# Kernel optimization log

Hardware: AMD Instinct MI355X
Metric: run time of the kernel (lower is better)

## Reference

```python
import jax, jax.numpy as jnp
import numpy as np

D, HEADS, HD, L, P, DFF = 256, 8, 32, 4, 4, 2048
B, NQ = 4, 900
SHAPES = [(128, 128), (64, 64), (32, 32), (16, 16)]
S = sum(h * w for h, w in SHAPES)


def setup_inputs():
    ks = iter(jax.random.split(jax.random.key(0), 20))
    rn = lambda *s: jax.random.normal(next(ks), s, jnp.float32) * 0.02
    cxcy = jax.random.uniform(next(ks), (B, NQ, 1, 2), minval=0.1, maxval=0.9)
    wh = jax.random.uniform(next(ks), (B, NQ, 1, 2), minval=0.05, maxval=0.3)
    ref = jnp.broadcast_to(jnp.concatenate([cxcy, wh], -1), (B, NQ, L, 4))
    starts = np.cumsum([0] + [h * w for h, w in SHAPES[:-1]])
    return dict(
        query=jax.random.normal(next(ks), (B, NQ, D), jnp.float32),
        query_pos=jax.random.normal(next(ks), (B, NQ, D), jnp.float32),
        reference_points=ref,
        input_flatten=jax.random.normal(next(ks), (B, S, D), jnp.float32),
        input_spatial_shapes=jnp.array(SHAPES, jnp.int32),
        input_level_start_index=jnp.array(starts, jnp.int32),
        sa_in_w=rn(3, D, D), sa_in_b=jnp.zeros((3, D)),
        sa_out_w=rn(D, D), sa_out_b=jnp.zeros((D,)),
        norm1_g=jnp.ones((D,)), norm1_b=jnp.zeros((D,)),
        value_w=rn(D, D), value_b=jnp.zeros((D,)),
        off_w=rn(D, HEADS * L * P * 2),
        off_b=jax.random.uniform(next(ks), (HEADS * L * P * 2,), minval=-1.0, maxval=1.0),
        aw_w=rn(D, HEADS * L * P), aw_b=jnp.zeros((HEADS * L * P,)),
        ca_out_w=rn(D, D), ca_out_b=jnp.zeros((D,)),
        norm2_g=jnp.ones((D,)), norm2_b=jnp.zeros((D,)),
        lin1_w=rn(D, DFF), lin1_b=jnp.zeros((DFF,)),
        lin2_w=rn(DFF, D), lin2_b=jnp.zeros((D,)),
        norm3_g=jnp.ones((D,)), norm3_b=jnp.zeros((D,)),
    )


def _ln(x, g, b, eps=1e-5):
    m = x.mean(-1, keepdims=True)
    v = ((x - m) ** 2).mean(-1, keepdims=True)
    return (x - m) * jax.lax.rsqrt(v + eps) * g + b


def _msdeform(q, input_flatten, ref, shapes, starts, value_w, value_b,
              off_w, off_b, aw_w, aw_b, out_w, out_b):
    Bq, Nq, _ = q.shape
    # value: (B, heads, S, head_dim)
    v = (input_flatten @ value_w + value_b).reshape(Bq, -1, HEADS, HD).transpose(0, 2, 1, 3)
    off = (q @ off_w + off_b).reshape(Bq, Nq, HEADS, L, P, 2).transpose(0, 2, 1, 3, 4, 5)
    aw = jax.nn.softmax((q @ aw_w + aw_b).reshape(Bq, Nq, HEADS, L * P), axis=-1)
    aw = aw.reshape(Bq, Nq, HEADS, L, P).transpose(0, 2, 1, 3, 4)  # (B,H,Nq,L,P)
    refc = ref[:, None, :, :, None, :]  # (B,1,Nq,L,1,4)
    # box refs: center + offset/P * wh * 0.5  (Deformable-DETR convention)
    loc = refc[..., :2] + off / P * refc[..., 2:] * 0.5  # (B,H,Nq,L,P,2)
    out = jnp.zeros((Bq, HEADS, Nq, HD), q.dtype)
    for l, (H, W) in enumerate(shapes):
        vl = jax.lax.dynamic_slice_in_dim(v, starts[l], H * W, axis=2)  # (B,H,HW,hd)
        x = loc[:, :, :, l, :, 0] * W - 0.5  # align_corners=False pixel coords
        y = loc[:, :, :, l, :, 1] * H - 0.5
        x0, y0 = jnp.floor(x), jnp.floor(y)
        dx, dy = x - x0, y - y0

        def g(xi, yi):
            valid = (xi >= 0) & (xi < W) & (yi >= 0) & (yi < H)  # zero padding
            idx = (jnp.clip(yi, 0, H - 1) * W + jnp.clip(xi, 0, W - 1)).astype(jnp.int32)
            gat = jnp.take_along_axis(vl, idx.reshape(Bq, HEADS, Nq * P, 1), axis=2)
            return gat.reshape(Bq, HEADS, Nq, P, HD) * valid[..., None]

        samp = (((1 - dx) * (1 - dy))[..., None] * g(x0, y0)
                + (dx * (1 - dy))[..., None] * g(x0 + 1, y0)
                + ((1 - dx) * dy)[..., None] * g(x0, y0 + 1)
                + (dx * dy)[..., None] * g(x0 + 1, y0 + 1))
        out = out + jnp.sum(aw[:, :, :, l, :, None] * samp, axis=3)
    return out.transpose(0, 2, 1, 3).reshape(Bq, Nq, D) @ out_w + out_b


def _layer(query, query_pos, reference_points, input_flatten, shapes, starts, p):
    Bq, Nq, _ = query.shape
    qk = query + query_pos
    heads = lambda x: x.reshape(Bq, Nq, HEADS, HD).transpose(0, 2, 1, 3)
    qh = heads(qk @ p['sa_in_w'][0] + p['sa_in_b'][0])
    kh = heads(qk @ p['sa_in_w'][1] + p['sa_in_b'][1])
    vh = heads(query @ p['sa_in_w'][2] + p['sa_in_b'][2])
    attn = jax.nn.softmax(jnp.einsum('bhqd,bhkd->bhqk', qh, kh) * (HD ** -0.5), axis=-1)
    sa = jnp.einsum('bhqk,bhkd->bhqd', attn, vh).transpose(0, 2, 1, 3).reshape(Bq, Nq, D)
    sa = sa @ p['sa_out_w'] + p['sa_out_b']
    x = _ln(query + sa, p['norm1_g'], p['norm1_b'])
    ca = _msdeform(x + query_pos, input_flatten, reference_points, shapes, starts,
                   p['value_w'], p['value_b'], p['off_w'], p['off_b'],
                   p['aw_w'], p['aw_b'], p['ca_out_w'], p['ca_out_b'])
    x = _ln(x + ca, p['norm2_g'], p['norm2_b'])
    ffn = jax.nn.relu(x @ p['lin1_w'] + p['lin1_b']) @ p['lin2_w'] + p['lin2_b']
    return _ln(x + ffn, p['norm3_g'], p['norm3_b'])


PNAMES = ['sa_in_w', 'sa_in_b', 'sa_out_w', 'sa_out_b', 'norm1_g', 'norm1_b',
          'value_w', 'value_b', 'off_w', 'off_b', 'aw_w', 'aw_b',
          'ca_out_w', 'ca_out_b', 'norm2_g', 'norm2_b',
          'lin1_w', 'lin1_b', 'lin2_w', 'lin2_b', 'norm3_g', 'norm3_b']


def reference(query, query_pos, reference_points, input_flatten,
              input_spatial_shapes, input_level_start_index,
              sa_in_w, sa_in_b, sa_out_w, sa_out_b, norm1_g, norm1_b,
              value_w, value_b, off_w, off_b, aw_w, aw_b,
              ca_out_w, ca_out_b, norm2_g, norm2_b,
              lin1_w, lin1_b, lin2_w, lin2_b, norm3_g, norm3_b):
    # spatial shapes / start indices are static structural metadata
    shapes = [(int(h), int(w)) for h, w in np.asarray(input_spatial_shapes)]
    starts = [int(s) for s in np.asarray(input_level_start_index)]
    p = dict(zip(PNAMES, (sa_in_w, sa_in_b, sa_out_w, sa_out_b, norm1_g, norm1_b,
                          value_w, value_b, off_w, off_b, aw_w, aw_b,
                          ca_out_w, ca_out_b, norm2_g, norm2_b,
                          lin1_w, lin1_b, lin2_w, lin2_b, norm3_g, norm3_b)))
    return _layer(query, query_pos, reference_points, input_flatten, shapes, starts, p)
```

## Files before the change

kernel.cpp:

```cpp
#include <hip/hip_runtime.h>
#include <hip/hip_bf16.h>

#define DD   256
#define NH   8
#define HDIM 32
#define LV   4
#define NP   4
#define DFF  2048
#define BB   4
#define NQQ  900
#define SS   21760

typedef __bf16 bf16x8 __attribute__((ext_vector_type(8)));
typedef __bf16 bf16x2 __attribute__((ext_vector_type(2)));
typedef float  f32x4  __attribute__((ext_vector_type(4)));

__device__ inline void stval(float* p, float v) { *p = v; }
__device__ inline void stval(__bf16* p, float v) { *p = (__bf16)v; }

__device__ __forceinline__ void gload16(const void* g, void* l) {
    __builtin_amdgcn_global_load_lds(
        (const __attribute__((address_space(1))) void*)g,
        (__attribute__((address_space(3))) void*)l, 16, 0, 0);
}

struct TPtrs {
    const float* s[10];
    __bf16* d[10];
};

__global__ void transp_all(TPtrs P) {
    const int Ks[10] = {256, 256, 256, 256, 256, 256, 256, 256, 256, 2048};
    const int Ns[10] = {256, 256, 256, 256, 256, 256, 128, 256, 2048, 256};
    const int tiles[10] = {64, 64, 64, 64, 64, 64, 32, 64, 512, 512};
    int t = blockIdx.x;
    int j = 0, base = 0;
    while (t >= base + tiles[j]) { base += tiles[j]; j++; }
    int lt = t - base;
    int K = Ks[j], N = Ns[j];
    int tn = N >> 5;
    int nb = (lt % tn) * 32, kb = (lt / tn) * 32;
    const float* W = P.s[j];
    __bf16* Wt = P.d[j];
    __shared__ float tbuf[32][33];
    for (int i = threadIdx.y; i < 32; i += 8)
        tbuf[i][threadIdx.x] = W[(size_t)(kb + i) * N + nb + threadIdx.x];
    __syncthreads();
    for (int i = threadIdx.y; i < 32; i += 8)
        Wt[(size_t)(nb + i) * K + kb + threadIdx.x] = (__bf16)tbuf[threadIdx.x][i];
}

#define BM 64
#define BN 64
#define BKK 64

template <typename AT, typename OT, int RELU, int NSUB, bool LNF>
__device__ __forceinline__ void gemm_body(
    int bx, int by, char* ldsraw,
    const AT* __restrict__ A, const float* __restrict__ A2,
    const __bf16* __restrict__ Wt,
    const float* __restrict__ bias, const float* __restrict__ bias2, int nsplit,
    const float* __restrict__ res, const float* __restrict__ lng,
    const float* __restrict__ lnb,
    OT* __restrict__ C, int M, int N, int K) {
    int tid = threadIdx.x;
    int lane = tid & 63;
    int wave = tid >> 6;
    int wr = wave >> 1, wc = wave & 1;
    int m0 = by * BM;
    int n0 = bx * (BN * NSUB);

    __bf16* As = (__bf16*)ldsraw;
    __bf16* Bs = (__bf16*)(ldsraw + BM * BKK * 2);
    float* rsum  = (float*)(ldsraw + BM * BKK * 2 + NSUB * BN * BKK * 2);
    float* rsum2 = rsum + 128;

    f32x4 acc[NSUB][2][2] = {};

    int srow = tid >> 2;
    int sq = tid & 3;
    int u0 = sq << 1;
    int p0 = (u0 ^ (srow & 7)) * 8;
    int p1 = ((u0 + 1) ^ (srow & 7)) * 8;
    int fr = lane & 15, gq = lane >> 4;

    for (int k0 = 0; k0 < K; k0 += BKK) {
        {
            int gm = m0 + srow;
            bf16x8 v0 = {}, v1 = {};
            if (gm < M) {
                if constexpr (sizeof(AT) == 4) {
                    const float* ap = (const float*)A + (size_t)gm * K + k0 + sq * 16;
                    f32x4 f0 = *(const f32x4*)(ap + 0);
                    f32x4 f1 = *(const f32x4*)(ap + 4);
                    f32x4 f2 = *(const f32x4*)(ap + 8);
                    f32x4 f3 = *(const f32x4*)(ap + 12);
                    if (A2) {
                        const float* ap2 = A2 + (size_t)gm * K + k0 + sq * 16;
                        f0 += *(const f32x4*)(ap2 + 0);
                        f1 += *(const f32x4*)(ap2 + 4);
                        f2 += *(const f32x4*)(ap2 + 8);
                        f3 += *(const f32x4*)(ap2 + 12);
                    }
#pragma unroll
                    for (int e = 0; e < 4; e++) {
                        v0[e] = (__bf16)f0[e]; v0[e + 4] = (__bf16)f1[e];
                        v1[e] = (__bf16)f2[e]; v1[e + 4] = (__bf16)f3[e];
                    }
                } else {
                    const __bf16* ap = (const __bf16*)A + (size_t)gm * K + k0 + sq * 16;
                    v0 = *(const bf16x8*)(ap);
                    v1 = *(const bf16x8*)(ap + 8);
                }
            }
            *(bf16x8*)(&As[srow * 64 + p0]) = v0;
            *(bf16x8*)(&As[srow * 64 + p1]) = v1;
        }
#pragma unroll
        for (int ns = 0; ns < NSUB; ns++) {
            int gn = n0 + ns * BN + srow;
            const __bf16* bp = Wt + (size_t)gn * K + k0 + sq * 16;
            bf16x8 w0 = *(const bf16x8*)(bp);
            bf16x8 w1 = *(const bf16x8*)(bp + 8);
            *(bf16x8*)(&Bs[ns * BN * BKK + srow * 64 + p0]) = w0;
            *(bf16x8*)(&Bs[ns * BN * BKK + srow * 64 + p1]) = w1;
        }
        __syncthreads();
#pragma unroll
        for (int ks = 0; ks < 2; ks++) {
            bf16x8 a[2];
#pragma unroll
            for (int i = 0; i < 2; i++) {
                int ma = wr * 32 + i * 16 + fr;
                a[i] = *(const bf16x8*)(&As[ma * 64 + ((ks * 4 + gq) ^ (ma & 7)) * 8]);
            }
#pragma unroll
            for (int ns = 0; ns < NSUB; ns++) {
                bf16x8 b[2];
#pragma unroll
                for (int j = 0; j < 2; j++) {
                    int nb = wc * 32 + j * 16 + fr;
                    b[j] = *(const bf16x8*)(&Bs[ns * BN * BKK + nb * 64 + ((ks * 4 + gq) ^ (nb & 7)) * 8]);
                }
#pragma unroll
                for (int i = 0; i < 2; i++)
#pragma unroll
                    for (int j = 0; j < 2; j++)
                        acc[ns][i][j] = __builtin_amdgcn_mfma_f32_16x16x32_bf16(a[i], b[j], acc[ns][i][j], 0, 0, 0);
            }
        }
        __syncthreads();
    }
    int orow = gq * 4;
    if constexpr (!LNF) {
#pragma unroll
        for (int ns = 0; ns < NSUB; ns++)
#pragma unroll
            for (int i = 0; i < 2; i++)
#pragma unroll
                for (int j = 0; j < 2; j++) {
                    int gn = n0 + ns * BN + wc * 32 + j * 16 + fr;
                    float bv = (gn < nsplit) ? bias[gn] : bias2[gn - nsplit];
#pragma unroll
                    for (int r = 0; r < 4; r++) {
                        int gm = m0 + wr * 32 + i * 16 + orow + r;
                        if (gm < M) {
                            float v = acc[ns][i][j][r] + bv;
                            if (RELU) v = fmaxf(v, 0.f);
                            stval(C + (size_t)gm * N + gn, v);
                        }
                    }
                }
    } else {
        float part[2][4] = {};
#pragma unroll
        for (int ns = 0; ns < NSUB; ns++)
#pragma unroll
            for (int i = 0; i < 2; i++)
#pragma unroll
                for (int j = 0; j < 2; j++) {
                    int gn = ns * BN + wc * 32 + j * 16 + fr;
                    float bv = bias[gn];
#pragma unroll
                    for (int r = 0; r < 4; r++) {
                        int gm = m0 + wr * 32 + i * 16 + orow + r;
                        float rv = (gm < M) ? res[(size_t)gm * 256 + gn] : 0.f;
                        float x = acc[ns][i][j][r] + bv + rv;
                        acc[ns][i][j][r] = x;
                        part[i][r] += x;
                    }
                }
#pragma unroll
        for (int i = 0; i < 2; i++)
#pragma unroll
            for (int r = 0; r < 4; r++) {
                float v = part[i][r];
                v += __shfl_xor(v, 1);
                v += __shfl_xor(v, 2);
                v += __shfl_xor(v, 4);
                v += __shfl_xor(v, 8);
                part[i][r] = v;
            }
        if (fr == 0) {
#pragma unroll
            for (int i = 0; i < 2; i++)
#pragma unroll
                for (int r = 0; r < 4; r++)
                    rsum[(wr * 32 + i * 16 + orow + r) * 2 + wc] = part[i][r];
        }
        __syncthreads();
        float mean[2][4];
#pragma unroll
        for (int i = 0; i < 2; i++)
#pragma unroll
            for (int r = 0; r < 4; r++) {
                int rl = wr * 32 + i * 16 + orow + r;
                mean[i][r] = (rsum[rl * 2] + rsum[rl * 2 + 1]) * (1.f / 256.f);
            }
        float p2[2][4] = {};
#pragma unroll
        for (int ns = 0; ns < NSUB; ns++)
#pragma unroll
            for (int i = 0; i < 2; i++)
#pragma unroll
                for (int j = 0; j < 2; j++)
#pragma unroll
                    for (int r = 0; r < 4; r++) {
                        float d = acc[ns][i][j][r] - mean[i][r];
                        p2[i][r] += d * d;
                    }
#pragma unroll
        for (int i = 0; i < 2; i++)
#pragma unroll
            for (int r = 0; r < 4; r++) {
                float v = p2[i][r];
                v += __shfl_xor(v, 1);
                v += __shfl_xor(v, 2);
                v += __shfl_xor(v, 4);
                v += __shfl_xor(v, 8);
                p2[i][r] = v;
            }
        if (fr == 0) {
#pragma unroll
            for (int i = 0; i < 2; i++)
#pragma unroll
                for (int r = 0; r < 4; r++)
                    rsum2[(wr * 32 + i * 16 + orow + r) * 2 + wc] = p2[i][r];
        }
        __syncthreads();
        float rstd[2][4];
#pragma unroll
        for (int i = 0; i < 2; i++)
#pragma unroll
            for (int r = 0; r < 4; r++) {
                int rl = wr * 32 + i * 16 + orow + r;
                float var = (rsum2[rl * 2] + rsum2[rl * 2 + 1]) * (1.f / 256.f);
                rstd[i][r] = rsqrtf(var + 1e-5f);
            }
#pragma unroll
        for (int ns = 0; ns < NSUB; ns++)
#pragma unroll
            for (int i = 0; i < 2; i++)
#pragma unroll
                for (int j = 0; j < 2; j++) {
                    int gn = ns * BN + wc * 32 + j * 16 + fr;
                    float gv = lng[gn], bev = lnb[gn];
#pragma unroll
                    for (int r = 0; r < 4; r++) {
                        int gm = m0 + wr * 32 + i * 16 + orow + r;
                        if (gm < M) {
                            float y = (acc[ns][i][j][r] - mean[i][r]) * rstd[i][r] * gv + bev;
                            stval(C + (size_t)gm * 256 + gn, y);
                        }
                    }
                }
    }
}

template <typename AT, typename OT, int RELU, int NSUB, bool LNF>
__global__ __launch_bounds__(256) void mfma_gemm(
    const AT* __restrict__ A, const float* __restrict__ A2,
    const __bf16* __restrict__ Wt,
    const float* __restrict__ bias, const float* __restrict__ bias2, int nsplit,
    const float* __restrict__ res, const float* __restrict__ lng,
    const float* __restrict__ lnb,
    OT* __restrict__ C, int M, int N, int K) {
    __shared__ __attribute__((aligned(16))) char lds[BM * BKK * 2 + NSUB * BN * BKK * 2 + (LNF ? 1024 : 0)];
    gemm_body<AT, OT, RELU, NSUB, LNF>(blockIdx.x, blockIdx.y, lds, A, A2, Wt,
                                       bias, bias2, nsplit, res, lng, lnb, C, M, N, K);
}

__device__ __forceinline__ void value_body(
    int bx, char* ldsraw,
    const float* __restrict__ A, const __bf16* __restrict__ Wt,
    const float* __restrict__ bias, __bf16* __restrict__ C) {
    int tid = threadIdx.x;
    int lane = tid & 63;
    int wave = tid >> 6;
    int fr = lane & 15, gq = lane >> 4;
    int m0 = bx * 64;

    __bf16* As = (__bf16*)ldsraw;
    __bf16* Bq = (__bf16*)(ldsraw + 16384);

    f32x4 acc[4][4] = {};

    int srow = tid >> 2;
    int sq = tid & 3;
    int u0 = sq << 1;
    int p0 = (u0 ^ (srow & 7)) * 8;
    int p1 = ((u0 + 1) ^ (srow & 7)) * 8;

    int c_row = lane >> 3;
    int c_u = lane & 7;
    int gu = c_u ^ c_row;
    const __bf16* bsrc0 = Wt + (size_t)(wave * 64 + c_row) * 256 + gu * 8;
    const float* aptr = A + (size_t)(m0 + srow) * 256 + sq * 16;

    f32x4 fa0 = *(const f32x4*)(aptr + 0);
    f32x4 fa1 = *(const f32x4*)(aptr + 4);
    f32x4 fa2 = *(const f32x4*)(aptr + 8);
    f32x4 fa3 = *(const f32x4*)(aptr + 12);
    __builtin_amdgcn_sched_barrier(0);
#pragma unroll
    for (int c = 0; c < 8; c++)
        gload16(bsrc0 + (size_t)c * 8 * 256, &Bq[wave * 4096 + c * 512]);
    asm volatile("s_waitcnt vmcnt(8)" ::: "memory");
    __builtin_amdgcn_sched_barrier(0);
    {
        bf16x8 v0, v1;
#pragma unroll
        for (int e = 0; e < 4; e++) {
            v0[e] = (__bf16)fa0[e]; v0[e + 4] = (__bf16)fa1[e];
            v1[e] = (__bf16)fa2[e]; v1[e + 4] = (__bf16)fa3[e];
        }
        *(bf16x8*)(&As[srow * 64 + p0]) = v0;
        *(bf16x8*)(&As[srow * 64 + p1]) = v1;
    }
    asm volatile("s_waitcnt lgkmcnt(0)" ::: "memory");
    __builtin_amdgcn_s_barrier();

#pragma unroll
    for (int step = 0; step < 4; step++) {
        int p = step & 1;
        if (step < 3) {
            const float* ap2 = aptr + (step + 1) * 64;
            fa0 = *(const f32x4*)(ap2 + 0);
            fa1 = *(const f32x4*)(ap2 + 4);
            fa2 = *(const f32x4*)(ap2 + 8);
            fa3 = *(const f32x4*)(ap2 + 12);
            __builtin_amdgcn_sched_barrier(0);
            const __bf16* bsrc = bsrc0 + (step + 1) * 64;
#pragma unroll
            for (int c = 0; c < 8; c++)
                gload16(bsrc + (size_t)c * 8 * 256, &Bq[((p ^ 1) * 4 + wave) * 4096 + c * 512]);
            asm volatile("s_waitcnt vmcnt(12)" ::: "memory");
        } else {
            asm volatile("s_waitcnt vmcnt(0)" ::: "memory");
        }
        __builtin_amdgcn_sched_barrier(0);
#pragma unroll
        for (int ks = 0; ks < 2; ks++) {
            bf16x8 a[4], b[4];
#pragma unroll
            for (int i = 0; i < 4; i++) {
                int ma = i * 16 + fr;
                a[i] = *(const bf16x8*)(&As[p * 4096 + ma * 64 + ((ks * 4 + gq) ^ (ma & 7)) * 8]);
                b[i] = *(const bf16x8*)(&Bq[(p * 4 + wave) * 4096 + ma * 64 + ((ks * 4 + gq) ^ (ma & 7)) * 8]);
            }
#pragma unroll
            for (int i = 0; i < 4; i++)
#pragma unroll
                for (int j = 0; j < 4; j++)
                    acc[i][j] = __builtin_amdgcn_mfma_f32_16x16x32_bf16(a[i], b[j], acc[i][j], 0, 0, 0);
        }
        if (step < 3) {
            asm volatile("s_waitcnt vmcnt(8)" ::: "memory");
            __builtin_amdgcn_sched_barrier(0);
            bf16x8 v0, v1;
#pragma unroll
            for (int e = 0; e < 4; e++) {
                v0[e] = (__bf16)fa0[e]; v0[e + 4] = (__bf16)fa1[e];
                v1[e] = (__bf16)fa2[e]; v1[e + 4] = (__bf16)fa3[e];
            }
            *(bf16x8*)(&As[(p ^ 1) * 4096 + srow * 64 + p0]) = v0;
            *(bf16x8*)(&As[(p ^ 1) * 4096 + srow * 64 + p1]) = v1;
            asm volatile("s_waitcnt lgkmcnt(0)" ::: "memory");
            __builtin_amdgcn_s_barrier();
        }
    }

#pragma unroll
    for (int i = 0; i < 4; i++)
#pragma unroll
        for (int j = 0; j < 4; j++) {
            int gn = wave * 64 + j * 16 + fr;
            float bv = bias[gn];
#pragma unroll
            for (int r = 0; r < 4; r++) {
                int gm = m0 + i * 16 + gq * 4 + r;
                C[(size_t)gm * 256 + gn] = (__bf16)(acc[i][j][r] + bv);
            }
        }
}

#define NVALB 1360
#define NQKB  228
#define NVB   228

__global__ __launch_bounds__(256) void fused_head(
    const float* __restrict__ input_flat, const __bf16* __restrict__ wt_val,
    const float* __restrict__ value_b, __bf16* __restrict__ vbig,
    const float* __restrict__ query, const float* __restrict__ query_pos,
    const __bf16* __restrict__ wt_q, const float* __restrict__ sa_in_b,
    __bf16* __restrict__ qkbuf, const __bf16* __restrict__ wt_v,
    __bf16* __restrict__ Vp, int M) {
    __shared__ __attribute__((aligned(16))) char lds[81920];
    int bx = blockIdx.x;
    if (bx < NVALB) {
        value_body(bx, lds, input_flat, wt_val, value_b, vbig);
    } else if (bx < NVALB + NQKB) {
        int b2 = bx - NVALB;
        gemm_body<float, __bf16, 0, 2, false>(b2 & 3, b2 >> 2, lds,
            query, query_pos, wt_q, sa_in_b, sa_in_b, 1 << 30,
            nullptr, nullptr, nullptr, qkbuf, M, 512, 256);
    } else {
        int b2 = bx - NVALB - NQKB;
        gemm_body<float, __bf16, 0, 1, false>(b2 & 3, b2 >> 2, lds,
            query, nullptr, wt_v, sa_in_b + 512, sa_in_b, 1 << 30,
            nullptr, nullptr, nullptr, Vp, M, 256, 256);
    }
}

__global__ void fillmark(float* o, int n, float v) {
    int i = blockIdx.x * blockDim.x + threadIdx.x;
    if (i < n) o[i] = v;
}

__global__ void ln_res(const float* a, const float* b,
                       const float* g, const float* be, float* o) {
    int row = blockIdx.x;
    int t = threadIdx.x;
    float x = a[(size_t)row * DD + t] + b[(size_t)row * DD + t];
    __shared__ float red[DD];
    red[t] = x;
    __syncthreads();
    for (int s = 128; s > 0; s >>= 1) {
        if (t < s) red[t] += red[t + s];
        __syncthreads();
    }
    float m = red[0] * (1.f / DD);
    __syncthreads();
    float d0 = x - m;
    red[t] = d0 * d0;
    __syncthreads();
    for (int s = 128; s > 0; s >>= 1) {
        if (t < s) red[t] += red[t + s];
        __syncthreads();
    }
    float v = red[0] * (1.f / DD);
    o[(size_t)row * DD + t] = d0 * rsqrtf(v + 1e-5f) * g[t] + be[t];
}

#define QT 64
#define KT 64
#define NT ((NQQ + KT - 1) / KT)
#define QKLD 512

__global__ __launch_bounds__(256) void sa_attn_mfma(
    const __bf16* __restrict__ QK, const __bf16* __restrict__ V,
    float* __restrict__ O) {
    int blk = blockIdx.x;
    int tq = blk % NT;
    int bh = blk / NT;
    int h = bh % NH;
    int b = bh / NH;
    int tid = threadIdx.x;
    int lane = tid & 63;
    int wave = tid >> 6;
    int fr = lane & 15, gq = lane >> 4;
    int q0 = tq * QT;

    __shared__ __attribute__((aligned(16))) __bf16 Ks[KT][56];
    __shared__ __attribute__((aligned(16))) __bf16 Vt[HDIM][72];
    __shared__ __attribute__((aligned(16))) __bf16 Ps[4][16][72];

    int qrow = q0 + wave * 16 + fr;
    bf16x8 aq = {};
    if (qrow < NQQ)
        aq = *(const bf16x8*)(QK + ((size_t)(b * NQQ + qrow)) * QKLD + h * HDIM + gq * 8);

    f32x4 o0 = {}, o1 = {};
    float m_r[4] = {-1e30f, -1e30f, -1e30f, -1e30f};
    float l_r[4] = {0.f, 0.f, 0.f, 0.f};
    const float scale = 0.17677669529663687f;

    for (int kt = 0; kt < NT; kt++) {
        int kv0 = kt * KT;
        {
            int r = tid >> 2;
            int c8 = (tid & 3) * 8;
            int kvr = kv0 + r;
            bf16x8 kv_ = {}, vv_ = {};
            if (kvr < NQQ) {
                kv_ = *(const bf16x8*)(QK + ((size_t)(b * NQQ + kvr)) * QKLD + 256 + h * HDIM + c8);
                vv_ = *(const bf16x8*)(V + ((size_t)(b * NQQ + kvr)) * DD + h * HDIM + c8);
            }
            *(bf16x8*)(&Ks[r][c8]) = kv_;
#pragma unroll
            for (int j = 0; j < 8; j++) Vt[c8 + j][r] = vv_[j];
        }
        __syncthreads();

        f32x4 s[4];
#pragma unroll
        for (int f = 0; f < 4; f++) {
            bf16x8 bk = *(const bf16x8*)(&Ks[f * 16 + fr][gq * 8]);
            f32x4 z = {};
            s[f] = __builtin_amdgcn_mfma_f32_16x16x32_bf16(aq, bk, z, 0, 0, 0);
        }
#pragma unroll
        for (int f = 0; f < 4; f++) {
            bool valid = (kv0 + f * 16 + fr) < NQQ;
#pragma unroll
            for (int r = 0; r < 4; r++)
                s[f][r] = valid ? s[f][r] * scale : -1e30f;
        }
        float sc_[4];
#pragma unroll
        for (int r = 0; r < 4; r++) {
            float v = fmaxf(fmaxf(s[0][r], s[1][r]), fmaxf(s[2][r], s[3][r]));
            v = fmaxf(v, __shfl_xor(v, 1));
            v = fmaxf(v, __shfl_xor(v, 2));
            v = fmaxf(v, __shfl_xor(v, 4));
            v = fmaxf(v, __shfl_xor(v, 8));
            float mn = fmaxf(m_r[r], v);
            sc_[r] = expf(m_r[r] - mn);
            m_r[r] = mn;
        }
        float rs[4] = {0.f, 0.f, 0.f, 0.f};
#pragma unroll
        for (int f = 0; f < 4; f++)
#pragma unroll
            for (int r = 0; r < 4; r++) {
                float e = expf(s[f][r] - m_r[r]);
                s[f][r] = e;
                rs[r] += e;
            }
#pragma unroll
        for (int r = 0; r < 4; r++) {
            float v = rs[r];
            v += __shfl_xor(v, 1);
            v += __shfl_xor(v, 2);
            v += __shfl_xor(v, 4);
            v += __shfl_xor(v, 8);
            l_r[r] = l_r[r] * sc_[r] + v;
            o0[r] *= sc_[r];
            o1[r] *= sc_[r];
        }
#pragma unroll
        for (int f = 0; f < 4; f++)
#pragma unroll
            for (int r = 0; r < 4; r++)
                Ps[wave][gq * 4 + r][f * 16 + fr] = (__bf16)s[f][r];
#pragma unroll
        for (int c = 0; c < 2; c++) {
            bf16x8 ap = *(const bf16x8*)(&Ps[wave][fr][c * 32 + gq * 8]);
            bf16x8 bv0 = *(const bf16x8*)(&Vt[fr][c * 32 + gq * 8]);
            bf16x8 bv1 = *(const bf16x8*)(&Vt[16 + fr][c * 32 + gq * 8]);
            o0 = __builtin_amdgcn_mfma_f32_16x16x32_bf16(ap, bv0, o0, 0, 0, 0);
            o1 = __builtin_amdgcn_mfma_f32_16x16x32_bf16(ap, bv1, o1, 0, 0, 0);
        }
        __syncthreads();
    }
#pragma unroll
    for (int r = 0; r < 4; r++) {
        int qr = q0 + wave * 16 + gq * 4 + r;
        if (qr < NQQ) {
            float inv = 1.f / l_r[r];
            O[((size_t)(b * NQQ + qr)) * DD + h * HDIM + fr] = o0[r] * inv;
            O[((size_t)(b * NQQ + qr)) * DD + h * HDIM + 16 + fr] = o1[r] * inv;
        }
    }
}

#define OAW 384

__global__ __launch_bounds__(256) void msdeform3(
    const __bf16* __restrict__ val, const __bf16* __restrict__ oa,
    const float* __restrict__ ref, float* __restrict__ out) {
    int tid = threadIdx.x;
    int row = blockIdx.x;
    int b_ = row / NQQ;

    __shared__ float sx[128], sy[128], sw[128];

    if (tid < 128) {
        int h = tid >> 4;
        int lp = tid & 15;
        int l = lp >> 2;
        float logit = (float)oa[(size_t)row * OAW + 256 + h * 16 + lp];
        float ox = (float)oa[(size_t)row * OAW + h * 32 + lp * 2];
        float oy = (float)oa[(size_t)row * OAW + h * 32 + lp * 2 + 1];
        const float* rp = ref + ((size_t)row * LV + l) * 4;
        float cx = rp[0], cy = rp[1], rw = rp[2], rh = rp[3];
        float mv = logit;
        mv = fmaxf(mv, __shfl_xor(mv, 1));
        mv = fmaxf(mv, __shfl_xor(mv, 2));
        mv = fmaxf(mv, __shfl_xor(mv, 4));
        mv = fmaxf(mv, __shfl_xor(mv, 8));
        float e = expf(logit - mv);
        float sum = e;
        sum += __shfl_xor(sum, 1);
        sum += __shfl_xor(sum, 2);
        sum += __shfl_xor(sum, 4);
        sum += __shfl_xor(sum, 8);
        int Wl = 128 >> l;
        float lx = cx + ox * (1.0f / NP) * rw * 0.5f;
        float ly = cy + oy * (1.0f / NP) * rh * 0.5f;
        sx[tid] = lx * Wl - 0.5f;
        sy[tid] = ly * Wl - 0.5f;
        sw[tid] = e / sum;
    }
    __syncthreads();

    int cpar = tid & 7;
    int dgrp = (tid >> 3) & 3;
    int h = tid >> 5;
    const int stt[4] = {0, 16384, 20480, 21504};
    const __bf16* vb = val + (size_t)b_ * SS * DD + h * HDIM + dgrp * 8;
    float facc[8] = {};
#pragma unroll
    for (int k = 0; k < 8; k++) {
        int combo = cpar * 8 + k;
        int lp = combo >> 2;
        int tap = combo & 3;
        int l = lp >> 2;
        int Wl = 128 >> l;
        int cidx = h * 16 + lp;
        float x = sx[cidx], y = sy[cidx], w = sw[cidx];
        float x0f = floorf(x), y0f = floorf(y);
        float dx = x - x0f, dy = y - y0f;
        int xi = (int)x0f + (tap & 1);
        int yi = (int)y0f + (tap >> 1);
        float wt = ((tap & 1) ? dx : 1.f - dx) * ((tap >> 1) ? dy : 1.f - dy) * w;
        if ((xi >= 0) & (xi < Wl) & (yi >= 0) & (yi < Wl)) {
            bf16x8 t = *(const bf16x8*)(vb + (size_t)(stt[l] + yi * Wl + xi) * DD);
#pragma unroll
            for (int e = 0; e < 8; e++) facc[e] += wt * (float)t[e];
        }
    }
#pragma unroll
    for (int e = 0; e < 8; e++) {
        facc[e] += __shfl_xor(facc[e], 1);
        facc[e] += __shfl_xor(facc[e], 2);
        facc[e] += __shfl_xor(facc[e], 4);
    }
    float v = facc[0];
#pragma unroll
    for (int e = 1; e < 8; e++) if (cpar == e) v = facc[e];
    out[(size_t)row * DD + tid] = v;
}

extern "C" void kernel_launch(void* const* d_in, const int* in_sizes, int n_in,
                              void* d_out, int out_size, void* d_ws, size_t ws_size,
                              hipStream_t stream) {
    const float* query      = (const float*)d_in[0];
    const float* query_pos  = (const float*)d_in[1];
    const float* refpts     = (const float*)d_in[2];
    const float* input_flat = (const float*)d_in[3];
    const float* sa_in_w    = (const float*)d_in[6];
    const float* sa_in_b    = (const float*)d_in[7];
    const float* sa_out_w   = (const float*)d_in[8];
    const float* sa_out_b   = (const float*)d_in[9];
    const float* norm1_g    = (const float*)d_in[10];
    const float* norm1_b    = (const float*)d_in[11];
    const float* value_w    = (const float*)d_in[12];
    const float* value_b    = (const float*)d_in[13];
    const float* off_w      = (const float*)d_in[14];
    const float* off_b      = (const float*)d_in[15];
    const float* aw_w       = (const float*)d_in[16];
    const float* aw_b       = (const float*)d_in[17];
    const float* ca_out_w   = (const float*)d_in[18];
    const float* ca_out_b   = (const float*)d_in[19];
    const float* norm2_g    = (const float*)d_in[20];
    const float* norm2_b    = (const float*)d_in[21];
    const float* lin1_w     = (const float*)d_in[22];
    const float* lin1_b     = (const float*)d_in[23];
    const float* lin2_w     = (const float*)d_in[24];
    const float* lin2_b     = (const float*)d_in[25];
    const float* norm3_g    = (const float*)d_in[26];
    const float* norm3_b    = (const float*)d_in[27];
    float* out = (float*)d_out;

    const int M = BB * NQQ;
    const int NE = M * DD;
    const size_t slotBytes = (size_t)NE * 4;
    const size_t wElems = 6 * 65536 + 32768 + 65536 + 2 * 524288;
    const size_t wBytes = wElems * 2;
    const size_t bigBytes = (size_t)BB * SS * DD * 2;
    const size_t needBytes = 3 * slotBytes + wBytes + bigBytes;
    if (ws_size < needBytes) {
        float mark = 1000.0f + (float)(ws_size >> 20);
        fillmark<<<(out_size + 255) / 256, 256, 0, stream>>>(out, out_size, mark);
        return;
    }

    char* wsb = (char*)d_ws;
    float* s0 = (float*)(wsb);
    float* s1 = (float*)(wsb + slotBytes);
    float* s2 = (float*)(wsb + 2 * slotBytes);
    __bf16* wb = (__bf16*)(wsb + 3 * slotBytes);
    __bf16* vbig = (__bf16*)(wsb + 3 * slotBytes + wBytes);

    __bf16* wt_q   = wb;
    __bf16* wt_k   = wb + 65536;
    __bf16* wt_v   = wb + 131072;
    __bf16* wt_sa  = wb + 196608;
    __bf16* wt_val = wb + 262144;
    __bf16* wt_off = wb + 327680;
    __bf16* wt_aw  = wb + 393216;
    __bf16* wt_ca  = wb + 425984;
    __bf16* wt_l1  = wb + 491520;
    __bf16* wt_l2  = wb + 1015808;

    TPtrs tp;
    tp.s[0] = sa_in_w;          tp.d[0] = wt_q;
    tp.s[1] = sa_in_w + 65536;  tp.d[1] = wt_k;
    tp.s[2] = sa_in_w + 131072; tp.d[2] = wt_v;
    tp.s[3] = sa_out_w;         tp.d[3] = wt_sa;
    tp.s[4] = value_w;          tp.d[4] = wt_val;
    tp.s[5] = off_w;            tp.d[5] = wt_off;
    tp.s[6] = aw_w;             tp.d[6] = wt_aw;
    tp.s[7] = ca_out_w;         tp.d[7] = wt_ca;
    tp.s[8] = lin1_w;           tp.d[8] = wt_l1;
    tp.s[9] = lin2_w;           tp.d[9] = wt_l2;
    transp_all<<<1504, dim3(32, 8), 0, stream>>>(tp);

    __bf16* qkbuf = (__bf16*)s1;
    __bf16* Vp = (__bf16*)s2;
    __bf16* oabuf = (__bf16*)s1;

    const int mt = (M + BM - 1) / BM;
    const int BIG = 1 << 30;

    fused_head<<<NVALB + NQKB + NVB, 256, 0, stream>>>(
        input_flat, wt_val, value_b, vbig,
        query, query_pos, wt_q, sa_in_b, qkbuf, wt_v, Vp, M);
    sa_attn_mfma<<<BB * NH * NT, 256, 0, stream>>>(qkbuf, Vp, s0);
    mfma_gemm<float, float, 0, 4, true><<<dim3(1, mt), 256, 0, stream>>>(
        s0, nullptr, wt_sa, sa_out_b, sa_out_b, BIG,
        query, norm1_g, norm1_b, s2, M, DD, DD);
    mfma_gemm<float, __bf16, 0, 1, false><<<dim3(6, mt), 256, 0, stream>>>(
        s2, query_pos, wt_off, off_b, aw_b, 256,
        nullptr, nullptr, nullptr, oabuf, M, OAW, DD);
    msdeform3<<<M, 256, 0, stream>>>(vbig, oabuf, refpts, s0);
    mfma_gemm<float, float, 0, 4, true><<<dim3(1, mt), 256, 0, stream>>>(
        s0, nullptr, wt_ca, ca_out_b, ca_out_b, BIG,
        s2, norm2_g, norm2_b, s1, M, DD, DD);
    mfma_gemm<float, __bf16, 1, 2, false><<<dim3(16, mt), 256, 0, stream>>>(
        s1, nullptr, wt_l1, lin1_b, lin1_b, BIG,
        nullptr, nullptr, nullptr, vbig, M, DFF, DD);
    mfma_gemm<__bf16, float, 0, 1, false><<<dim3(4, mt), 256, 0, stream>>>(
        vbig, nullptr, wt_l2, lin2_b, lin2_b, BIG,
        nullptr, nullptr, nullptr, s0, M, DD, DFF);
    ln_res<<<M, DD, 0, stream>>>(s1, s0, norm3_g, norm3_b, out);
}
```

Measured before the change: 203.8 us.

## Co-schedule self-attention with value projection and fuse final LayerNorm into lin2

Moves the large value-projection GEMM out of the head kernel and launches it in one kernel alongside the self-attention blocks. Value projection then overlaps with attention, and the QKV projection becomes a small standalone kernel. The lin2 GEMM now uses the full-row variant with residual-plus-LayerNorm epilogue, which removes the separate ln_res kernel and its extra pass over the data. The trade-offs are reduced column parallelism for lin2 (one column tile across K=2048) and the 80KB LDS allocation now applying to attention blocks, which may limit occupancy.

```diff
diff --git a/kernel.cpp b/kernel.cpp
--- a/kernel.cpp
+++ b/kernel.cpp
@@ -404,73 +404,15 @@
         }
 }
 
-#define NVALB 1360
-#define NQKB  228
-#define NVB   228
-
-__global__ __launch_bounds__(256) void fused_head(
-    const float* __restrict__ input_flat, const __bf16* __restrict__ wt_val,
-    const float* __restrict__ value_b, __bf16* __restrict__ vbig,
-    const float* __restrict__ query, const float* __restrict__ query_pos,
-    const __bf16* __restrict__ wt_q, const float* __restrict__ sa_in_b,
-    __bf16* __restrict__ qkbuf, const __bf16* __restrict__ wt_v,
-    __bf16* __restrict__ Vp, int M) {
-    __shared__ __attribute__((aligned(16))) char lds[81920];
-    int bx = blockIdx.x;
-    if (bx < NVALB) {
-        value_body(bx, lds, input_flat, wt_val, value_b, vbig);
-    } else if (bx < NVALB + NQKB) {
-        int b2 = bx - NVALB;
-        gemm_body<float, __bf16, 0, 2, false>(b2 & 3, b2 >> 2, lds,
-            query, query_pos, wt_q, sa_in_b, sa_in_b, 1 << 30,
-            nullptr, nullptr, nullptr, qkbuf, M, 512, 256);
-    } else {
-        int b2 = bx - NVALB - NQKB;
-        gemm_body<float, __bf16, 0, 1, false>(b2 & 3, b2 >> 2, lds,
-            query, nullptr, wt_v, sa_in_b + 512, sa_in_b, 1 << 30,
-            nullptr, nullptr, nullptr, Vp, M, 256, 256);
-    }
-}
-
-__global__ void fillmark(float* o, int n, float v) {
-    int i = blockIdx.x * blockDim.x + threadIdx.x;
-    if (i < n) o[i] = v;
-}
-
-__global__ void ln_res(const float* a, const float* b,
-                       const float* g, const float* be, float* o) {
-    int row = blockIdx.x;
-    int t = threadIdx.x;
-    float x = a[(size_t)row * DD + t] + b[(size_t)row * DD + t];
-    __shared__ float red[DD];
-    red[t] = x;
-    __syncthreads();
-    for (int s = 128; s > 0; s >>= 1) {
-        if (t < s) red[t] += red[t + s];
-        __syncthreads();
-    }
-    float m = red[0] * (1.f / DD);
-    __syncthreads();
-    float d0 = x - m;
-    red[t] = d0 * d0;
-    __syncthreads();
-    for (int s = 128; s > 0; s >>= 1) {
-        if (t < s) red[t] += red[t + s];
-        __syncthreads();
-    }
-    float v = red[0] * (1.f / DD);
-    o[(size_t)row * DD + t] = d0 * rsqrtf(v + 1e-5f) * g[t] + be[t];
-}
-
 #define QT 64
 #define KT 64
 #define NT ((NQQ + KT - 1) / KT)
 #define QKLD 512
 
-__global__ __launch_bounds__(256) void sa_attn_mfma(
+__device__ __forceinline__ void attn_body(
+    int blk, char* ldsraw,
     const __bf16* __restrict__ QK, const __bf16* __restrict__ V,
     float* __restrict__ O) {
-    int blk = blockIdx.x;
     int tq = blk % NT;
     int bh = blk / NT;
     int h = bh % NH;
@@ -481,9 +423,9 @@
     int fr = lane & 15, gq = lane >> 4;
     int q0 = tq * QT;
 
-    __shared__ __attribute__((aligned(16))) __bf16 Ks[KT][56];
-    __shared__ __attribute__((aligned(16))) __bf16 Vt[HDIM][72];
-    __shared__ __attribute__((aligned(16))) __bf16 Ps[4][16][72];
+    __bf16* Ks = (__bf16*)ldsraw;
+    __bf16* Vt = (__bf16*)(ldsraw + 7168);
+    __bf16* Ps = (__bf16*)(ldsraw + 11776);
 
     int qrow = q0 + wave * 16 + fr;
     bf16x8 aq = {};
@@ -506,16 +448,16 @@
                 kv_ = *(const bf16x8*)(QK + ((size_t)(b * NQQ + kvr)) * QKLD + 256 + h * HDIM + c8);
                 vv_ = *(const bf16x8*)(V + ((size_t)(b * NQQ + kvr)) * DD + h * HDIM + c8);
             }
-            *(bf16x8*)(&Ks[r][c8]) = kv_;
-#pragma unroll
-            for (int j = 0; j < 8; j++) Vt[c8 + j][r] = vv_[j];
+            *(bf16x8*)(&Ks[r * 56 + c8]) = kv_;
+#pragma unroll
+            for (int j = 0; j < 8; j++) Vt[(c8 + j) * 72 + r] = vv_[j];
         }
         __syncthreads();
 
         f32x4 s[4];
 #pragma unroll
         for (int f = 0; f < 4; f++) {
-            bf16x8 bk = *(const bf16x8*)(&Ks[f * 16 + fr][gq * 8]);
+            bf16x8 bk = *(const bf16x8*)(&Ks[(f * 16 + fr) * 56 + gq * 8]);
             f32x4 z = {};
             s[f] = __builtin_amdgcn_mfma_f32_16x16x32_bf16(aq, bk, z, 0, 0, 0);
         }
@@ -562,12 +504,12 @@
         for (int f = 0; f < 4; f++)
 #pragma unroll
             for (int r = 0; r < 4; r++)
-                Ps[wave][gq * 4 + r][f * 16 + fr] = (__bf16)s[f][r];
+                Ps[(wave * 16 + gq * 4 + r) * 72 + f * 16 + fr] = (__bf16)s[f][r];
 #pragma unroll
         for (int c = 0; c < 2; c++) {
-            bf16x8 ap = *(const bf16x8*)(&Ps[wave][fr][c * 32 + gq * 8]);
-            bf16x8 bv0 = *(const bf16x8*)(&Vt[fr][c * 32 + gq * 8]);
-            bf16x8 bv1 = *(const bf16x8*)(&Vt[16 + fr][c * 32 + gq * 8]);
+            bf16x8 ap = *(const bf16x8*)(&Ps[(wave * 16 + fr) * 72 + c * 32 + gq * 8]);
+            bf16x8 bv0 = *(const bf16x8*)(&Vt[fr * 72 + c * 32 + gq * 8]);
+            bf16x8 bv1 = *(const bf16x8*)(&Vt[(16 + fr) * 72 + c * 32 + gq * 8]);
             o0 = __builtin_amdgcn_mfma_f32_16x16x32_bf16(ap, bv0, o0, 0, 0, 0);
             o1 = __builtin_amdgcn_mfma_f32_16x16x32_bf16(ap, bv1, o1, 0, 0, 0);
         }
@@ -582,6 +524,49 @@
             O[((size_t)(b * NQQ + qr)) * DD + h * HDIM + 16 + fr] = o1[r] * inv;
         }
     }
+}
+
+#define NATT  (BB * NH * NT)
+#define NVALB 1360
+#define NQKB  228
+#define NVB   228
+
+__global__ __launch_bounds__(256) void qkv_proj(
+    const float* __restrict__ query, const float* __restrict__ query_pos,
+    const __bf16* __restrict__ wt_q, const float* __restrict__ sa_in_b,
+    __bf16* __restrict__ qkbuf, const __bf16* __restrict__ wt_v,
+    __bf16* __restrict__ Vp, int M) {
+    __shared__ __attribute__((aligned(16))) char lds[24576];
+    int bx = blockIdx.x;
+    if (bx < NQKB) {
+        gemm_body<float, __bf16, 0, 2, false>(bx & 3, bx >> 2, lds,
+            query, query_pos, wt_q, sa_in_b, sa_in_b, 1 << 30,
+            nullptr, nullptr, nullptr, qkbuf, M, 512, 256);
+    } else {
+        int b2 = bx - NQKB;
+        gemm_body<float, __bf16, 0, 1, false>(b2 & 3, b2 >> 2, lds,
+            query, nullptr, wt_v, sa_in_b + 512, sa_in_b, 1 << 30,
+            nullptr, nullptr, nullptr, Vp, M, 256, 256);
+    }
+}
+
+__global__ __launch_bounds__(256) void fused_av(
+    const __bf16* __restrict__ qkbuf, const __bf16* __restrict__ Vp,
+    float* __restrict__ attnO,
+    const float* __restrict__ input_flat, const __bf16* __restrict__ wt_val,
+    const float* __restrict__ value_b, __bf16* __restrict__ vbig) {
+    __shared__ __attribute__((aligned(16))) char lds[81920];
+    int bx = blockIdx.x;
+    if (bx < NATT) {
+        attn_body(bx, lds, qkbuf, Vp, attnO);
+    } else {
+        value_body(bx - NATT, lds, input_flat, wt_val, value_b, vbig);
+    }
+}
+
+__global__ void fillmark(float* o, int n, float v) {
+    int i = blockIdx.x * blockDim.x + threadIdx.x;
+    if (i < n) o[i] = v;
 }
 
 #define OAW 384
@@ -744,10 +729,10 @@
     const int mt = (M + BM - 1) / BM;
     const int BIG = 1 << 30;
 
-    fused_head<<<NVALB + NQKB + NVB, 256, 0, stream>>>(
-        input_flat, wt_val, value_b, vbig,
+    qkv_proj<<<NQKB + NVB, 256, 0, stream>>>(
         query, query_pos, wt_q, sa_in_b, qkbuf, wt_v, Vp, M);
-    sa_attn_mfma<<<BB * NH * NT, 256, 0, stream>>>(qkbuf, Vp, s0);
+    fused_av<<<NATT + NVALB, 256, 0, stream>>>(
+        qkbuf, Vp, s0, input_flat, wt_val, value_b, vbig);
     mfma_gemm<float, float, 0, 4, true><<<dim3(1, mt), 256, 0, stream>>>(
         s0, nullptr, wt_sa, sa_out_b, sa_out_b, BIG,
         query, norm1_g, norm1_b, s2, M, DD, DD);
@@ -761,8 +746,7 @@
     mfma_gemm<float, __bf16, 1, 2, false><<<dim3(16, mt), 256, 0, stream>>>(
         s1, nullptr, wt_l1, lin1_b, lin1_b, BIG,
         nullptr, nullptr, nullptr, vbig, M, DFF, DD);
-    mfma_gemm<__bf16, float, 0, 1, false><<<dim3(4, mt), 256, 0, stream>>>(
+    mfma_gemm<__bf16, float, 0, 4, true><<<dim3(1, mt), 256, 0, stream>>>(
         vbig, nullptr, wt_l2, lin2_b, lin2_b, BIG,
-        nullptr, nullptr, nullptr, s0, M, DD, DFF);
-    ln_res<<<M, DD, 0, stream>>>(s1, s0, norm3_g, norm3_b, out);
-}
+        s1, norm3_g, norm3_b, out, M, DD, DFF);
+}
```

After: 212.9 us. +4.5%, slower.
